# Performance work log

Hardware: AMD Instinct MI355X
Metric: run time of the kernel (lower is better)

## Reference

```python
import jax, jax.numpy as jnp
import numpy as np

HID, OUT, VOC, MEM, MDIM, OPN = 2048, 4096, 4096, 4096, 64, 5

def setup_inputs() -> dict:
    key = jax.random.key(0)
    ks = jax.random.split(key, 16)
    s = 0.02
    return {
        "input": jax.random.normal(ks[0], (1, 1, VOC), jnp.float32),
        "hidden0": jax.random.normal(ks[1], (1, 1, HID), jnp.float32),
        "memory": jax.random.normal(ks[2], (MEM, MDIM), jnp.float32),
        "W_ih": jax.random.normal(ks[3], (HID, VOC), jnp.float32) * s,
        "b_ih": jax.random.normal(ks[4], (HID,), jnp.float32) * s,
        "W_hh": jax.random.normal(ks[5], (HID, HID), jnp.float32) * s,
        "b_hh": jax.random.normal(ks[6], (HID,), jnp.float32) * s,
        "Wm_w": jax.random.normal(ks[7], (HID, MDIM), jnp.float32) * s,
        "Wm_b": jax.random.normal(ks[8], (HID,), jnp.float32) * s,
        "Wy_w": jax.random.normal(ks[9], (OUT, HID), jnp.float32) * s,
        "Wy_b": jax.random.normal(ks[10], (OUT,), jnp.float32) * s,
        "Wn_w": jax.random.normal(ks[11], (MDIM, HID), jnp.float32) * s,
        "Wn_b": jax.random.normal(ks[12], (MDIM,), jnp.float32) * s,
        "Wa_w": jax.random.normal(ks[13], (OPN, HID), jnp.float32) * s,
        "Wa_b": jax.random.normal(ks[14], (OPN,), jnp.float32) * s,
    }

def reference(input, hidden0, memory, W_ih, b_ih, W_hh, b_hh, Wm_w, Wm_b,
              Wy_w, Wy_b, Wn_w, Wn_b, Wa_w, Wa_b):
    # hidden_bar = W_m(memory[0]) + hidden0 ; shapes: (HID,)
    h_bar = memory[0] @ Wm_w.T + Wm_b + hidden0[0, 0]
    # single-step, single-layer tanh RNN
    x = input[0, 0]  # (VOC,)
    h = jnp.tanh(x @ W_ih.T + b_ih + h_bar @ W_hh.T + b_hh)  # (HID,)
    ht = h.reshape(1, 1, HID)
    output = jax.nn.sigmoid(h @ Wy_w.T + Wy_b).reshape(1, 1, OUT)
    a = jax.nn.softmax(h @ Wa_w.T + Wa_b)  # (5,) action weights
    new_elt = jax.nn.sigmoid(h @ Wn_w.T + Wn_b)  # (MDIM,)
    # Permutation matmuls expressed as exact index shifts:
    left = jnp.roll(memory, -1, axis=0)          # leftmove @ memory
    right = jnp.roll(memory, 1, axis=0)          # rightmove @ memory
    leftinv = right.at[0].set(0.0)               # rightmove with row 0 zeroed
    rightinv = left.at[MEM - 1].set(0.0)         # leftmove with last row zeroed
    mem = (left * a[0] + right * a[1] + memory * a[2]
           + leftinv * a[3] + rightinv * a[4])
    # simple_addition @ new_elt adds new_elt into row 0 only
    mem = mem.at[0].add(new_elt)
    return (output, ht, mem)
```

## Files before the change

kernel.cpp:

```cpp
#include <hip/hip_runtime.h>
#include <hip/hip_bf16.h>

#define HID 2048
#define OUTN 4096
#define VOC 4096
#define MEMN 4096
#define MDIM 64
#define OPN 5

static __device__ __forceinline__ float wave_reduce(float v) {
    #pragma unroll
    for (int off = 32; off > 0; off >>= 1) v += __shfl_down(v, off, 64);
    return v;
}

static __device__ __forceinline__ float block_reduce(float v, float* red) {
    int lane = threadIdx.x & 63;
    int wid = threadIdx.x >> 6;
    v = wave_reduce(v);
    if (lane == 0) red[wid] = v;
    __syncthreads();
    return red[0] + red[1] + red[2] + red[3];
}

__global__ __launch_bounds__(256) void k_hbar(
        const float* __restrict__ Wm_w,
        const float* __restrict__ Wm_b,
        const float* __restrict__ memory,
        const float* __restrict__ hidden0,
        float* __restrict__ h_bar) {
    int wave = (blockIdx.x * blockDim.x + threadIdx.x) >> 6;
    int lane = threadIdx.x & 63;
    if (wave >= HID) return;
    float v = Wm_w[(size_t)wave * MDIM + lane] * memory[lane];
    v = wave_reduce(v);
    if (lane == 0)
        h_bar[wave] = v + Wm_b[wave] + hidden0[wave];
}

__global__ __launch_bounds__(256) void k_hidden(
        const float* __restrict__ W_ih,
        const float* __restrict__ x,
        const float* __restrict__ b_ih,
        const float* __restrict__ W_hh,
        const float* __restrict__ b_hh,
        const float* __restrict__ h_bar,
        float* __restrict__ h,
        float* __restrict__ ht_out) {
    __shared__ float red[4];
    int row = blockIdx.x;
    int tid = threadIdx.x;
    float acc = 0.f;
    const float* wrow = W_ih + (size_t)row * VOC;
    #pragma unroll
    for (int p = 0; p < VOC / (256 * 4); ++p) {
        int k = (p * 256 + tid) * 4;
        float4 w = *(const float4*)(wrow + k);
        float4 xv = *(const float4*)(x + k);
        acc += w.x * xv.x + w.y * xv.y + w.z * xv.z + w.w * xv.w;
    }
    const float* wrow2 = W_hh + (size_t)row * HID;
    #pragma unroll
    for (int p = 0; p < HID / (256 * 4); ++p) {
        int k = (p * 256 + tid) * 4;
        float4 w = *(const float4*)(wrow2 + k);
        float4 hv = *(const float4*)(h_bar + k);
        acc += w.x * hv.x + w.y * hv.y + w.z * hv.z + w.w * hv.w;
    }
    float s = block_reduce(acc, red);
    if (tid == 0) {
        float hv = tanhf(s + b_ih[row] + b_hh[row]);
        h[row] = hv;
        ht_out[row] = hv;
    }
}

__global__ __launch_bounds__(256) void k_heads(
        const float* __restrict__ Wy_w,
        const float* __restrict__ Wy_b,
        const float* __restrict__ Wn_w,
        const float* __restrict__ Wn_b,
        const float* __restrict__ Wa_w,
        const float* __restrict__ Wa_b,
        const float* __restrict__ h,
        float* __restrict__ out,
        float* __restrict__ new_elt,
        float* __restrict__ wa_logits) {
    __shared__ float red[4];
    int row = blockIdx.x;
    int tid = threadIdx.x;
    const float* wrow;
    if (row < OUTN)             wrow = Wy_w + (size_t)row * HID;
    else if (row < OUTN + MDIM) wrow = Wn_w + (size_t)(row - OUTN) * HID;
    else                        wrow = Wa_w + (size_t)(row - OUTN - MDIM) * HID;
    float acc = 0.f;
    #pragma unroll
    for (int p = 0; p < HID / (256 * 4); ++p) {
        int k = (p * 256 + tid) * 4;
        float4 w = *(const float4*)(wrow + k);
        float4 hv = *(const float4*)(h + k);
        acc += w.x * hv.x + w.y * hv.y + w.z * hv.z + w.w * hv.w;
    }
    float s = block_reduce(acc, red);
    if (tid == 0) {
        if (row < OUTN) {
            float v = s + Wy_b[row];
            out[row] = 1.f / (1.f + expf(-v));
        } else if (row < OUTN + MDIM) {
            int r = row - OUTN;
            float v = s + Wn_b[r];
            new_elt[r] = 1.f / (1.f + expf(-v));
        } else {
            int r = row - OUTN - MDIM;
            wa_logits[r] = s + Wa_b[r];
        }
    }
}

__global__ __launch_bounds__(256) void k_mem(
        const float* __restrict__ m,
        const float* __restrict__ wa,
        const float* __restrict__ new_elt,
        float* __restrict__ mem_out) {
    int idx = blockIdx.x * blockDim.x + threadIdx.x;
    if (idx >= MEMN * MDIM) return;
    float l0 = wa[0], l1 = wa[1], l2 = wa[2], l3 = wa[3], l4 = wa[4];
    float mx = fmaxf(fmaxf(fmaxf(l0, l1), fmaxf(l2, l3)), l4);
    float e0 = expf(l0 - mx), e1 = expf(l1 - mx), e2 = expf(l2 - mx),
          e3 = expf(l3 - mx), e4 = expf(l4 - mx);
    float inv = 1.f / (e0 + e1 + e2 + e3 + e4);
    float a0 = e0 * inv, a1 = e1 * inv, a2 = e2 * inv, a3 = e3 * inv, a4 = e4 * inv;

    int r = idx >> 6, c = idx & (MDIM - 1);
    float mc = m[idx];
    float mp = m[(size_t)((r + 1) & (MEMN - 1)) * MDIM + c];
    float mm = m[(size_t)((r - 1) & (MEMN - 1)) * MDIM + c];
    float cp = a0 + (r < MEMN - 1 ? a4 : 0.f);
    float cm = a1 + (r > 0 ? a3 : 0.f);
    float v = cp * mp + cm * mm + a2 * mc;
    if (r == 0) v += new_elt[c];
    mem_out[idx] = v;
}

extern "C" void kernel_launch(void* const* d_in, const int* in_sizes, int n_in,
                              void* d_out, int out_size, void* d_ws, size_t ws_size,
                              hipStream_t stream) {
    const float* input   = (const float*)d_in[0];
    const float* hidden0 = (const float*)d_in[1];
    const float* memory  = (const float*)d_in[2];
    const float* W_ih    = (const float*)d_in[3];
    const float* b_ih    = (const float*)d_in[4];
    const float* W_hh    = (const float*)d_in[5];
    const float* b_hh    = (const float*)d_in[6];
    const float* Wm_w    = (const float*)d_in[7];
    const float* Wm_b    = (const float*)d_in[8];
    const float* Wy_w    = (const float*)d_in[9];
    const float* Wy_b    = (const float*)d_in[10];
    const float* Wn_w    = (const float*)d_in[11];
    const float* Wn_b    = (const float*)d_in[12];
    const float* Wa_w    = (const float*)d_in[13];
    const float* Wa_b    = (const float*)d_in[14];

    float* ws      = (float*)d_ws;
    float* h_bar   = ws;
    float* h       = ws + 2048;
    float* wa      = ws + 4096;
    float* new_elt = ws + 4104;

    float* out_f = (float*)d_out;
    float* ht_f  = (float*)d_out + OUTN;
    float* mem_f = (float*)d_out + OUTN + HID;

    k_hbar<<<HID / 4, 256, 0, stream>>>(Wm_w, Wm_b, memory, hidden0, h_bar);
    k_hidden<<<HID, 256, 0, stream>>>(W_ih, input, b_ih, W_hh, b_hh,
                                      h_bar, h, ht_f);
    int rows3 = OUTN + MDIM + OPN;
    k_heads<<<rows3, 256, 0, stream>>>(Wy_w, Wy_b, Wn_w, Wn_b,
                                       Wa_w, Wa_b, h, out_f,
                                       new_elt, wa);
    k_mem<<<(MEMN * MDIM) / 256, 256, 0, stream>>>(memory, wa, new_elt, mem_f);
}
```

Before: 137.1 us.

## Restructure RNN step: fuse h_bar with W_ih GEMV, merge heads with memory update

Moves the W_ih·x GEMV, which does not depend on h_bar, into the first kernel alongside the h_bar computation, so the second kernel only streams W_hh. The separate memory-update kernel is folded into the heads kernel. There, 128 extra blocks each recompute the Wn/Wa projections redundantly into shared memory and then update a slice of memory with float4 loads. This cuts one launch and the workspace round trip for the action and new_elt vectors. The cost is 128 redundant passes over the 69-row Wn/Wa weights.

```diff
diff --git a/kernel.cpp b/kernel.cpp
--- a/kernel.cpp
+++ b/kernel.cpp
@@ -1,5 +1,4 @@
 #include <hip/hip_runtime.h>
-#include <hip/hip_bf16.h>
 
 #define HID 2048
 #define OUTN 4096
@@ -23,59 +22,68 @@
     return red[0] + red[1] + red[2] + red[3];
 }
 
-__global__ __launch_bounds__(256) void k_hbar(
+__global__ __launch_bounds__(256) void k1_ih_hbar(
+        const float* __restrict__ W_ih,
+        const float* __restrict__ x,
+        const float* __restrict__ b_ih,
+        const float* __restrict__ b_hh,
         const float* __restrict__ Wm_w,
         const float* __restrict__ Wm_b,
         const float* __restrict__ memory,
         const float* __restrict__ hidden0,
-        float* __restrict__ h_bar) {
-    int wave = (blockIdx.x * blockDim.x + threadIdx.x) >> 6;
-    int lane = threadIdx.x & 63;
-    if (wave >= HID) return;
-    float v = Wm_w[(size_t)wave * MDIM + lane] * memory[lane];
-    v = wave_reduce(v);
-    if (lane == 0)
-        h_bar[wave] = v + Wm_b[wave] + hidden0[wave];
-}
-
-__global__ __launch_bounds__(256) void k_hidden(
-        const float* __restrict__ W_ih,
-        const float* __restrict__ x,
-        const float* __restrict__ b_ih,
+        float* __restrict__ h_bar,
+        float* __restrict__ s_pre) {
+    __shared__ float red[4];
+    int row = blockIdx.x;
+    int tid = threadIdx.x;
+
+    if (tid < 64) {
+        float v = Wm_w[(size_t)row * MDIM + tid] * memory[tid];
+        v = wave_reduce(v);
+        if (tid == 0) h_bar[row] = v + Wm_b[row] + hidden0[row];
+    }
+
+    const float* wrow = W_ih + (size_t)row * VOC;
+    float acc = 0.f;
+    #pragma unroll
+    for (int p = 0; p < VOC / (256 * 4); ++p) {
+        int k = (p * 256 + tid) * 4;
+        float4 w  = *(const float4*)(wrow + k);
+        float4 xv = *(const float4*)(x + k);
+        acc += w.x * xv.x + w.y * xv.y + w.z * xv.z + w.w * xv.w;
+    }
+    float s = block_reduce(acc, red);
+    if (tid == 0) s_pre[row] = s + b_ih[row] + b_hh[row];
+}
+
+__global__ __launch_bounds__(256) void k2_hidden(
         const float* __restrict__ W_hh,
-        const float* __restrict__ b_hh,
         const float* __restrict__ h_bar,
+        const float* __restrict__ s_pre,
         float* __restrict__ h,
         float* __restrict__ ht_out) {
     __shared__ float red[4];
     int row = blockIdx.x;
     int tid = threadIdx.x;
+    const float* wrow = W_hh + (size_t)row * HID;
     float acc = 0.f;
-    const float* wrow = W_ih + (size_t)row * VOC;
-    #pragma unroll
-    for (int p = 0; p < VOC / (256 * 4); ++p) {
-        int k = (p * 256 + tid) * 4;
-        float4 w = *(const float4*)(wrow + k);
-        float4 xv = *(const float4*)(x + k);
-        acc += w.x * xv.x + w.y * xv.y + w.z * xv.z + w.w * xv.w;
-    }
-    const float* wrow2 = W_hh + (size_t)row * HID;
     #pragma unroll
     for (int p = 0; p < HID / (256 * 4); ++p) {
         int k = (p * 256 + tid) * 4;
-        float4 w = *(const float4*)(wrow2 + k);
+        float4 w  = *(const float4*)(wrow + k);
         float4 hv = *(const float4*)(h_bar + k);
         acc += w.x * hv.x + w.y * hv.y + w.z * hv.z + w.w * hv.w;
     }
     float s = block_reduce(acc, red);
     if (tid == 0) {
-        float hv = tanhf(s + b_ih[row] + b_hh[row]);
+        float hv = tanhf(s + s_pre[row]);
         h[row] = hv;
         ht_out[row] = hv;
     }
 }
 
-__global__ __launch_bounds__(256) void k_heads(
+#define STB 128
+__global__ __launch_bounds__(256) void k3_heads_mem(
         const float* __restrict__ Wy_w,
         const float* __restrict__ Wy_b,
         const float* __restrict__ Wn_w,
@@ -83,63 +91,83 @@
         const float* __restrict__ Wa_w,
         const float* __restrict__ Wa_b,
         const float* __restrict__ h,
-        float* __restrict__ out,
-        float* __restrict__ new_elt,
-        float* __restrict__ wa_logits) {
+        const float* __restrict__ memory,
+        float* __restrict__ out_f,
+        float* __restrict__ mem_f) {
     __shared__ float red[4];
-    int row = blockIdx.x;
+    __shared__ float sm[MDIM + OPN];
+    int bid = blockIdx.x;
     int tid = threadIdx.x;
-    const float* wrow;
-    if (row < OUTN)             wrow = Wy_w + (size_t)row * HID;
-    else if (row < OUTN + MDIM) wrow = Wn_w + (size_t)(row - OUTN) * HID;
-    else                        wrow = Wa_w + (size_t)(row - OUTN - MDIM) * HID;
-    float acc = 0.f;
-    #pragma unroll
-    for (int p = 0; p < HID / (256 * 4); ++p) {
-        int k = (p * 256 + tid) * 4;
-        float4 w = *(const float4*)(wrow + k);
-        float4 hv = *(const float4*)(h + k);
-        acc += w.x * hv.x + w.y * hv.y + w.z * hv.z + w.w * hv.w;
-    }
-    float s = block_reduce(acc, red);
-    if (tid == 0) {
-        if (row < OUTN) {
-            float v = s + Wy_b[row];
-            out[row] = 1.f / (1.f + expf(-v));
-        } else if (row < OUTN + MDIM) {
-            int r = row - OUTN;
-            float v = s + Wn_b[r];
-            new_elt[r] = 1.f / (1.f + expf(-v));
-        } else {
-            int r = row - OUTN - MDIM;
-            wa_logits[r] = s + Wa_b[r];
-        }
-    }
-}
-
-__global__ __launch_bounds__(256) void k_mem(
-        const float* __restrict__ m,
-        const float* __restrict__ wa,
-        const float* __restrict__ new_elt,
-        float* __restrict__ mem_out) {
-    int idx = blockIdx.x * blockDim.x + threadIdx.x;
-    if (idx >= MEMN * MDIM) return;
-    float l0 = wa[0], l1 = wa[1], l2 = wa[2], l3 = wa[3], l4 = wa[4];
+
+    if (bid < OUTN) {
+        const float* wrow = Wy_w + (size_t)bid * HID;
+        float acc = 0.f;
+        #pragma unroll
+        for (int p = 0; p < HID / (256 * 4); ++p) {
+            int k = (p * 256 + tid) * 4;
+            float4 w  = *(const float4*)(wrow + k);
+            float4 hv = *(const float4*)(h + k);
+            acc += w.x * hv.x + w.y * hv.y + w.z * hv.z + w.w * hv.w;
+        }
+        float s = block_reduce(acc, red);
+        if (tid == 0) out_f[bid] = 1.f / (1.f + expf(-(s + Wy_b[bid])));
+        return;
+    }
+
+    int sb = bid - OUTN;
+    int lane = tid & 63;
+    int wid = tid >> 6;
+
+    for (int r = wid; r < MDIM + OPN; r += 4) {
+        const float* wrow = (r < MDIM) ? (Wn_w + (size_t)r * HID)
+                                       : (Wa_w + (size_t)(r - MDIM) * HID);
+        float acc = 0.f;
+        #pragma unroll
+        for (int p = 0; p < HID / (64 * 4); ++p) {
+            int k = (p * 64 + lane) * 4;
+            float4 w  = *(const float4*)(wrow + k);
+            float4 hv = *(const float4*)(h + k);
+            acc += w.x * hv.x + w.y * hv.y + w.z * hv.z + w.w * hv.w;
+        }
+        acc = wave_reduce(acc);
+        if (lane == 0) {
+            if (r < MDIM) sm[r] = 1.f / (1.f + expf(-(acc + Wn_b[r])));
+            else          sm[r] = acc + Wa_b[r - MDIM];
+        }
+    }
+    __syncthreads();
+
+    float l0 = sm[MDIM + 0], l1 = sm[MDIM + 1], l2 = sm[MDIM + 2],
+          l3 = sm[MDIM + 3], l4 = sm[MDIM + 4];
     float mx = fmaxf(fmaxf(fmaxf(l0, l1), fmaxf(l2, l3)), l4);
     float e0 = expf(l0 - mx), e1 = expf(l1 - mx), e2 = expf(l2 - mx),
           e3 = expf(l3 - mx), e4 = expf(l4 - mx);
     float inv = 1.f / (e0 + e1 + e2 + e3 + e4);
-    float a0 = e0 * inv, a1 = e1 * inv, a2 = e2 * inv, a3 = e3 * inv, a4 = e4 * inv;
-
-    int r = idx >> 6, c = idx & (MDIM - 1);
-    float mc = m[idx];
-    float mp = m[(size_t)((r + 1) & (MEMN - 1)) * MDIM + c];
-    float mm = m[(size_t)((r - 1) & (MEMN - 1)) * MDIM + c];
-    float cp = a0 + (r < MEMN - 1 ? a4 : 0.f);
-    float cm = a1 + (r > 0 ? a3 : 0.f);
-    float v = cp * mp + cm * mm + a2 * mc;
-    if (r == 0) v += new_elt[c];
-    mem_out[idx] = v;
+    float a0 = e0 * inv, a1 = e1 * inv, a2 = e2 * inv, a3 = e3 * inv,
+          a4 = e4 * inv;
+
+    #pragma unroll
+    for (int v = 0; v < 2; ++v) {
+        int e = sb * 2048 + (v * 256 + tid) * 4;
+        int r = e >> 6, c = e & (MDIM - 1);
+        const float4 mc = *(const float4*)(memory + e);
+        const float4 mp = *(const float4*)(memory + (((r + 1) & (MEMN - 1)) << 6) + c);
+        const float4 mm = *(const float4*)(memory + (((r - 1) & (MEMN - 1)) << 6) + c);
+        float cp = a0 + (r < MEMN - 1 ? a4 : 0.f);
+        float cm = a1 + (r > 0 ? a3 : 0.f);
+        float4 o;
+        o.x = cp * mp.x + cm * mm.x + a2 * mc.x;
+        o.y = cp * mp.y + cm * mm.y + a2 * mc.y;
+        o.z = cp * mp.z + cm * mm.z + a2 * mc.z;
+        o.w = cp * mp.w + cm * mm.w + a2 * mc.w;
+        if (r == 0) {
+            o.x += sm[c + 0];
+            o.y += sm[c + 1];
+            o.z += sm[c + 2];
+            o.w += sm[c + 3];
+        }
+        *(float4*)(mem_f + e) = o;
+    }
 }
 
 extern "C" void kernel_launch(void* const* d_in, const int* in_sizes, int n_in,
@@ -161,22 +189,20 @@
     const float* Wa_w    = (const float*)d_in[13];
     const float* Wa_b    = (const float*)d_in[14];
 
-    float* ws      = (float*)d_ws;
-    float* h_bar   = ws;
-    float* h       = ws + 2048;
-    float* wa      = ws + 4096;
-    float* new_elt = ws + 4104;
+    float* ws    = (float*)d_ws;
+    float* h_bar = ws;
+    float* s_pre = ws + 2048;
+    float* h     = ws + 4096;
 
     float* out_f = (float*)d_out;
     float* ht_f  = (float*)d_out + OUTN;
     float* mem_f = (float*)d_out + OUTN + HID;
 
-    k_hbar<<<HID / 4, 256, 0, stream>>>(Wm_w, Wm_b, memory, hidden0, h_bar);
-    k_hidden<<<HID, 256, 0, stream>>>(W_ih, input, b_ih, W_hh, b_hh,
-                                      h_bar, h, ht_f);
-    int rows3 = OUTN + MDIM + OPN;
-    k_heads<<<rows3, 256, 0, stream>>>(Wy_w, Wy_b, Wn_w, Wn_b,
-                                       Wa_w, Wa_b, h, out_f,
-                                       new_elt, wa);
-    k_mem<<<(MEMN * MDIM) / 256, 256, 0, stream>>>(memory, wa, new_elt, mem_f);
-}
+    k1_ih_hbar<<<HID, 256, 0, stream>>>(W_ih, input, b_ih, b_hh,
+                                        Wm_w, Wm_b, memory, hidden0,
+                                        h_bar, s_pre);
+    k2_hidden<<<HID, 256, 0, stream>>>(W_hh, h_bar, s_pre, h, ht_f);
+    k3_heads_mem<<<OUTN + STB, 256, 0, stream>>>(Wy_w, Wy_b, Wn_w, Wn_b,
+                                                 Wa_w, Wa_b, h, memory,
+                                                 out_f, mem_f);
+}
```

New measurement: 162.3 us. +18.4%, slower.
